# Optimization experiments

Measured on AMD Instinct MI355X. Metric: run time of the kernel, lower is better.

Reference implementation:

```python
import jax, jax.numpy as jnp
import numpy as np

N_SRC0, N_DST0, N_DST1 = 100000, 20000, 4000
E0, E1 = 640000, 128000
IN_F, HID_F, OUT_F = 512, 512, 256


def _graph_conv(x_src, src, dst, W, b, n_src, n_dst):
    """DGL GraphConv, norm='both': D_out^{-1/2} A D_in^{-1/2} X W + b."""
    ones_e = jnp.ones(src.shape[0], x_src.dtype)
    out_deg = jnp.maximum(jax.ops.segment_sum(ones_e, src, num_segments=n_src), 1.0)
    in_deg = jnp.maximum(jax.ops.segment_sum(ones_e, dst, num_segments=n_dst), 1.0)
    h = x_src * (out_deg ** -0.5)[:, None]          # [n_src, F] pre-normalize
    agg = jax.ops.segment_sum(h[src], dst, num_segments=n_dst)  # gather -> scatter-add
    agg = agg * (in_deg ** -0.5)[:, None]           # [n_dst, F]
    return agg @ W + b


def setup_inputs() -> dict:
    key = jax.random.key(0)
    ks = jax.random.split(key, 8)
    x = jax.random.normal(ks[0], (N_SRC0, IN_F), jnp.float32)
    src0 = jax.random.randint(ks[1], (E0,), 0, N_SRC0)
    dst0 = jax.random.randint(ks[2], (E0,), 0, N_DST0)
    src1 = jax.random.randint(ks[3], (E1,), 0, N_DST0)
    dst1 = jax.random.randint(ks[4], (E1,), 0, N_DST1)
    W1 = jax.random.normal(ks[5], (IN_F, HID_F), jnp.float32) * (IN_F ** -0.5)
    b1 = jnp.zeros((HID_F,), jnp.float32)
    W2 = jax.random.normal(ks[6], (HID_F, OUT_F), jnp.float32) * (HID_F ** -0.5)
    b2 = jnp.zeros((OUT_F,), jnp.float32)
    return {"x": x, "src0": src0, "dst0": dst0, "src1": src1, "dst1": dst1,
            "W1": W1, "b1": b1, "W2": W2, "b2": b2,
            "n_src0": N_SRC0, "n_dst0": N_DST0, "n_dst1": N_DST1}


def reference(x, src0, dst0, src1, dst1, W1, b1, W2, b2, n_src0, n_dst0, n_dst1):
    h = jax.nn.relu(_graph_conv(x, src0, dst0, W1, b1, n_src0, n_dst0))
    out = jax.nn.relu(_graph_conv(h, src1, dst1, W2, b2, n_dst0, n_dst1))
    return out
```

## Files before the change

### kernel.cpp

```cpp
#include <hip/hip_runtime.h>

typedef unsigned short ushort_t;
typedef unsigned int uint_t;
typedef __attribute__((ext_vector_type(8))) short s8v;
typedef __attribute__((ext_vector_type(4))) float f4v;

#define NS0 100000
#define ND0 20000
#define ND1 4000
#define E0  640000
#define E1  128000
#define F   512
#define OF  256
#define NCNT (NS0 + ND0 + ND0 + ND1)
#define SB  96

__device__ __forceinline__ ushort_t f2b(float f) {
    uint_t u = __float_as_uint(f);
    uint_t r = (u + 0x7fffu + ((u >> 16) & 1u)) >> 16;
    return (ushort_t)r;
}
__device__ __forceinline__ float b2f_lo(uint_t u) { return __uint_as_float(u << 16); }
__device__ __forceinline__ float b2f_hi(uint_t u) { return __uint_as_float(u & 0xffff0000u); }

__global__ __launch_bounds__(256) void bucket_fill(const int* __restrict__ src0, const int* __restrict__ dst0,
                                                   const int* __restrict__ src1, const int* __restrict__ dst1,
                                                   int* __restrict__ cntOut0, int* __restrict__ cntIn0,
                                                   int* __restrict__ cntOut1, int* __restrict__ cntIn1,
                                                   int* __restrict__ es0, int* __restrict__ es1) {
    int b = blockIdx.x;
    if (b < 625) {
        int e = (b * 256 + threadIdx.x) * 4;
        int4 s = *(const int4*)(src0 + e);
        int4 d = *(const int4*)(dst0 + e);
        atomicAdd(&cntOut0[s.x], 1);
        atomicAdd(&cntOut0[s.y], 1);
        atomicAdd(&cntOut0[s.z], 1);
        atomicAdd(&cntOut0[s.w], 1);
        int p0 = atomicAdd(&cntIn0[d.x], 1);
        int p1 = atomicAdd(&cntIn0[d.y], 1);
        int p2 = atomicAdd(&cntIn0[d.z], 1);
        int p3 = atomicAdd(&cntIn0[d.w], 1);
        es0[d.x * SB + min(p0, SB - 1)] = s.x;
        es0[d.y * SB + min(p1, SB - 1)] = s.y;
        es0[d.z * SB + min(p2, SB - 1)] = s.z;
        es0[d.w * SB + min(p3, SB - 1)] = s.w;
    } else {
        int e = ((b - 625) * 256 + threadIdx.x) * 4;
        int4 s = *(const int4*)(src1 + e);
        int4 d = *(const int4*)(dst1 + e);
        atomicAdd(&cntOut1[s.x], 1);
        atomicAdd(&cntOut1[s.y], 1);
        atomicAdd(&cntOut1[s.z], 1);
        atomicAdd(&cntOut1[s.w], 1);
        int p0 = atomicAdd(&cntIn1[d.x], 1);
        int p1 = atomicAdd(&cntIn1[d.y], 1);
        int p2 = atomicAdd(&cntIn1[d.z], 1);
        int p3 = atomicAdd(&cntIn1[d.w], 1);
        es1[d.x * SB + min(p0, SB - 1)] = s.x;
        es1[d.y * SB + min(p1, SB - 1)] = s.y;
        es1[d.z * SB + min(p2, SB - 1)] = s.z;
        es1[d.w * SB + min(p3, SB - 1)] = s.w;
    }
}

#define WBLK ((F * F + F * OF) / 256)
#define XBLK (NS0 * 128 / 256)
__global__ __launch_bounds__(256) void conv_wx(const float* __restrict__ W1, const float* __restrict__ W2,
                                               ushort_t* __restrict__ wt1, ushort_t* __restrict__ wt2,
                                               const float* __restrict__ x, ushort_t* __restrict__ xb) {
    if (blockIdx.x < WBLK) {
        int i = blockIdx.x * 256 + threadIdx.x;
        if (i < F * F) {
            int k = i >> 9, n = i & (F - 1);
            wt1[n * F + k] = f2b(W1[i]);
        } else {
            int j = i - F * F;
            int k = j >> 8, n = j & (OF - 1);
            wt2[n * F + k] = f2b(W2[j]);
        }
        return;
    }
    int i = (blockIdx.x - WBLK) * 256 + threadIdx.x;
    if (i >= NS0 * 128) return;
    f4v v = __builtin_nontemporal_load(((const f4v*)x) + i);
    uint2 o;
    o.x = (uint_t)f2b(v.x) | ((uint_t)f2b(v.y) << 16);
    o.y = (uint_t)f2b(v.z) | ((uint_t)f2b(v.w) << 16);
    ((uint2*)xb)[i] = o;
}

__device__ __forceinline__ void fma8(float* acc, uint4 u, float sc) {
    acc[0] += b2f_lo(u.x) * sc; acc[1] += b2f_hi(u.x) * sc;
    acc[2] += b2f_lo(u.y) * sc; acc[3] += b2f_hi(u.y) * sc;
    acc[4] += b2f_lo(u.z) * sc; acc[5] += b2f_hi(u.z) * sc;
    acc[6] += b2f_lo(u.w) * sc; acc[7] += b2f_hi(u.w) * sc;
}
__device__ __forceinline__ void add8(float* acc, uint4 u) {
    acc[0] += b2f_lo(u.x); acc[1] += b2f_hi(u.x);
    acc[2] += b2f_lo(u.y); acc[3] += b2f_hi(u.y);
    acc[4] += b2f_lo(u.z); acc[5] += b2f_hi(u.z);
    acc[6] += b2f_lo(u.w); acc[7] += b2f_hi(u.w);
}

__global__ __launch_bounds__(256) void agg_l1(const ushort_t* __restrict__ X, const int* __restrict__ es,
                                              const int* __restrict__ cntIn, const int* __restrict__ cntOut,
                                              ushort_t* __restrict__ out, int ndst) {
    int d = __builtin_amdgcn_readfirstlane(blockIdx.x * 4 + (threadIdx.x >> 6));
    if (d >= ndst) return;
    int lane = threadIdx.x & 63;
    int n = min(cntIn[d], SB);
    const int* ed = es + (size_t)d * SB;
    const uint4* Xv = (const uint4*)X;
    float acc[8] = {0.f, 0.f, 0.f, 0.f, 0.f, 0.f, 0.f, 0.f};
    int i = 0;
    for (; i + 8 <= n; i += 8) {
        int sv[8];
        #pragma unroll
        for (int j = 0; j < 8; ++j) sv[j] = ed[i + j];
        uint4 u[8];
        #pragma unroll
        for (int j = 0; j < 8; ++j) u[j] = Xv[(size_t)sv[j] * 64 + lane];
        float scv[8];
        #pragma unroll
        for (int j = 0; j < 8; ++j) scv[j] = rsqrtf(fmaxf((float)cntOut[sv[j]], 1.0f));
        #pragma unroll
        for (int j = 0; j < 8; ++j) fma8(acc, u[j], scv[j]);
    }
    for (; i < n; ++i) {
        int s = ed[i];
        float sc = rsqrtf(fmaxf((float)cntOut[s], 1.0f));
        fma8(acc, Xv[(size_t)s * 64 + lane], sc);
    }
    float sc = rsqrtf(fmaxf((float)n, 1.0f));
    uint4 o;
    o.x = (uint_t)f2b(acc[0] * sc) | ((uint_t)f2b(acc[1] * sc) << 16);
    o.y = (uint_t)f2b(acc[2] * sc) | ((uint_t)f2b(acc[3] * sc) << 16);
    o.z = (uint_t)f2b(acc[4] * sc) | ((uint_t)f2b(acc[5] * sc) << 16);
    o.w = (uint_t)f2b(acc[6] * sc) | ((uint_t)f2b(acc[7] * sc) << 16);
    ((uint4*)out)[(size_t)d * 64 + lane] = o;
}

__global__ __launch_bounds__(256) void agg_l2(const ushort_t* __restrict__ X, const int* __restrict__ es,
                                              const int* __restrict__ cntIn, ushort_t* __restrict__ out,
                                              int ndst) {
    int d = __builtin_amdgcn_readfirstlane(blockIdx.x * 4 + (threadIdx.x >> 6));
    if (d >= ndst) return;
    int lane = threadIdx.x & 63;
    int n = min(cntIn[d], SB);
    const int* ed = es + (size_t)d * SB;
    const uint4* Xv = (const uint4*)X;
    float acc[8] = {0.f, 0.f, 0.f, 0.f, 0.f, 0.f, 0.f, 0.f};
    int i = 0;
    for (; i + 16 <= n; i += 16) {
        uint4 u[16];
        #pragma unroll
        for (int j = 0; j < 16; ++j) u[j] = Xv[(size_t)ed[i + j] * 64 + lane];
        #pragma unroll
        for (int j = 0; j < 16; ++j) add8(acc, u[j]);
    }
    for (; i + 4 <= n; i += 4) {
        uint4 u[4];
        #pragma unroll
        for (int j = 0; j < 4; ++j) u[j] = Xv[(size_t)ed[i + j] * 64 + lane];
        #pragma unroll
        for (int j = 0; j < 4; ++j) add8(acc, u[j]);
    }
    for (; i < n; ++i) add8(acc, Xv[(size_t)ed[i] * 64 + lane]);
    float sc = rsqrtf(fmaxf((float)n, 1.0f));
    uint4 o;
    o.x = (uint_t)f2b(acc[0] * sc) | ((uint_t)f2b(acc[1] * sc) << 16);
    o.y = (uint_t)f2b(acc[2] * sc) | ((uint_t)f2b(acc[3] * sc) << 16);
    o.z = (uint_t)f2b(acc[4] * sc) | ((uint_t)f2b(acc[5] * sc) << 16);
    o.w = (uint_t)f2b(acc[6] * sc) | ((uint_t)f2b(acc[7] * sc) << 16);
    ((uint4*)out)[(size_t)d * 64 + lane] = o;
}

template <typename OutT>
__global__ __launch_bounds__(256) void gemm128(const ushort_t* __restrict__ A, const ushort_t* __restrict__ BT,
                                               const float* __restrict__ bias, const int* __restrict__ rowCnt,
                                               OutT* __restrict__ C, int M, int N, int K) {
    __shared__ __align__(16) ushort_t As[128 * 64];
    __shared__ __align__(16) ushort_t Bs[128 * 64];
    int tid = threadIdx.x;
    int lane = tid & 63, w = tid >> 6;
    int m16 = lane & 15, quad = lane >> 4;
    int wm = w & 1, wn = w >> 1;
    int bm = blockIdx.x * 128, bn = blockIdx.y * 128;
    f4v acc[4][4] = {};
    for (int k0 = 0; k0 < K; k0 += 64) {
        #pragma unroll
        for (int i = 0; i < 4; ++i) {
            int c = i * 256 + tid;
            int row = c >> 3, seg = (c & 7) * 8;
            int ra = bm + row; if (ra >= M) ra = M - 1;
            __builtin_amdgcn_global_load_lds(
                (const __attribute__((address_space(1))) uint_t*)(A + (size_t)ra * K + k0 + seg),
                (__attribute__((address_space(3))) uint_t*)(As + (size_t)c * 8), 16, 0, 0);
        }
        #pragma unroll
        for (int i = 0; i < 4; ++i) {
            int c = i * 256 + tid;
            int row = c >> 3, seg = (c & 7) * 8;
            int rb = bn + row;
            __builtin_amdgcn_global_load_lds(
                (const __attribute__((address_space(1))) uint_t*)(BT + (size_t)rb * K + k0 + seg),
                (__attribute__((address_space(3))) uint_t*)(Bs + (size_t)c * 8), 16, 0, 0);
        }
        __syncthreads();
        #pragma unroll
        for (int kc = 0; kc < 2; ++kc) {
            int co = kc * 32 + quad * 8;
            s8v af[4], bf[4];
            #pragma unroll
            for (int m = 0; m < 4; ++m)
                af[m] = *(const s8v*)&As[(wm * 64 + m * 16 + m16) * 64 + co];
            #pragma unroll
            for (int nn = 0; nn < 4; ++nn)
                bf[nn] = *(const s8v*)&Bs[(wn * 64 + nn * 16 + m16) * 64 + co];
            #pragma unroll
            for (int m = 0; m < 4; ++m)
                #pragma unroll
                for (int nn = 0; nn < 4; ++nn)
                    acc[m][nn] = __builtin_amdgcn_mfma_f32_16x16x32_bf16(af[m], bf[nn], acc[m][nn], 0, 0, 0);
        }
        __syncthreads();
    }
    #pragma unroll
    for (int m = 0; m < 4; ++m) {
        #pragma unroll
        for (int rr = 0; rr < 4; ++rr) {
            int row = bm + wm * 64 + m * 16 + quad * 4 + rr;
            if (row < M) {
                float rs = rowCnt ? rsqrtf(fmaxf((float)rowCnt[row], 1.0f)) : 1.0f;
                #pragma unroll
                for (int nn = 0; nn < 4; ++nn) {
                    int col = bn + wn * 64 + nn * 16 + m16;
                    float v = fmaxf(acc[m][nn][rr] + bias[col], 0.0f) * rs;
                    if (sizeof(OutT) == 2)
                        ((ushort_t*)C)[(size_t)row * N + col] = f2b(v);
                    else
                        ((float*)C)[(size_t)row * N + col] = v;
                }
            }
        }
    }
}

extern "C" void kernel_launch(void* const* d_in, const int* in_sizes, int n_in,
                              void* d_out, int out_size, void* d_ws, size_t ws_size,
                              hipStream_t stream) {
    (void)in_sizes; (void)n_in; (void)out_size; (void)ws_size;
    const float* x    = (const float*)d_in[0];
    const int*   src0 = (const int*)d_in[1];
    const int*   dst0 = (const int*)d_in[2];
    const int*   src1 = (const int*)d_in[3];
    const int*   dst1 = (const int*)d_in[4];
    const float* W1   = (const float*)d_in[5];
    const float* b1   = (const float*)d_in[6];
    const float* W2   = (const float*)d_in[7];
    const float* b2   = (const float*)d_in[8];
    float* out = (float*)d_out;

    char* p = (char*)d_ws;
    auto alloc = [&](size_t bytes) { char* q = p; p += (bytes + 255) & ~(size_t)255; return q; };
    int*      cnt  = (int*)alloc((size_t)NCNT * 4);
    int*      es0  = (int*)alloc((size_t)ND0 * SB * 4);
    int*      es1  = (int*)alloc((size_t)ND1 * SB * 4);
    ushort_t* wt1  = (ushort_t*)alloc((size_t)F * F * 2);
    ushort_t* wt2  = (ushort_t*)alloc((size_t)OF * F * 2);
    ushort_t* agg0 = (ushort_t*)alloc((size_t)ND0 * F * 2);
    ushort_t* h    = (ushort_t*)alloc((size_t)ND0 * F * 2);
    ushort_t* agg1 = (ushort_t*)alloc((size_t)ND1 * F * 2);
    ushort_t* xb   = (ushort_t*)alloc((size_t)NS0 * F * 2);

    int* cntOut0 = cnt;
    int* cntIn0  = cnt + NS0;
    int* cntOut1 = cnt + NS0 + ND0;
    int* cntIn1  = cnt + NS0 + ND0 + ND0;

    (void)hipMemsetAsync(cnt, 0, (size_t)NCNT * 4, stream);

    bucket_fill<<<750, 256, 0, stream>>>(src0, dst0, src1, dst1,
                                         cntOut0, cntIn0, cntOut1, cntIn1, es0, es1);

    conv_wx<<<WBLK + XBLK, 256, 0, stream>>>(W1, W2, wt1, wt2, x, xb);

    agg_l1<<<(ND0 + 3) / 4, 256, 0, stream>>>(xb, es0, cntIn0, cntOut0, agg0, ND0);

    gemm128<ushort_t><<<dim3((ND0 + 127) / 128, F / 128), 256, 0, stream>>>(
        agg0, wt1, b1, cntOut1, h, ND0, F, F);

    agg_l2<<<(ND1 + 3) / 4, 256, 0, stream>>>(h, es1, cntIn1, agg1, ND1);

    gemm128<float><<<dim3((ND1 + 127) / 128, OF / 128), 256, 0, stream>>>(
        agg1, wt2, b2, nullptr, out, ND1, OF, F);
}
```

Before: 532.7 us.

## Merge bucket fill and conversion kernels; prefetch next edge indices in agg_l1

Combines the edge bucketing kernel and the weight/feature bf16 conversion kernel into a single launch, so the atomic-heavy bucketing blocks and the bandwidth-bound x conversion blocks can run concurrently and one launch gap goes away. The agg_l1 main loop now loads the next 8 source indices before accumulating the current batch, which shortens the dependency between the index load and the gather. The bounds check on the x conversion was removed because the grid divides evenly. Register pressure in agg_l1 rises slightly.

```diff
diff --git a/kernel.cpp b/kernel.cpp
--- a/kernel.cpp
+++ b/kernel.cpp
@@ -15,6 +15,9 @@
 #define NCNT (NS0 + ND0 + ND0 + ND1)
 #define SB  96
 
+#define WBLK ((F * F + F * OF) / 256)
+#define XBLK (NS0 * 128 / 256)
+
 __device__ __forceinline__ ushort_t f2b(float f) {
     uint_t u = __float_as_uint(f);
     uint_t r = (u + 0x7fffu + ((u >> 16) & 1u)) >> 16;
@@ -23,11 +26,14 @@
 __device__ __forceinline__ float b2f_lo(uint_t u) { return __uint_as_float(u << 16); }
 __device__ __forceinline__ float b2f_hi(uint_t u) { return __uint_as_float(u & 0xffff0000u); }
 
-__global__ __launch_bounds__(256) void bucket_fill(const int* __restrict__ src0, const int* __restrict__ dst0,
-                                                   const int* __restrict__ src1, const int* __restrict__ dst1,
-                                                   int* __restrict__ cntOut0, int* __restrict__ cntIn0,
-                                                   int* __restrict__ cntOut1, int* __restrict__ cntIn1,
-                                                   int* __restrict__ es0, int* __restrict__ es1) {
+__global__ __launch_bounds__(256) void prep(const int* __restrict__ src0, const int* __restrict__ dst0,
+                                            const int* __restrict__ src1, const int* __restrict__ dst1,
+                                            int* __restrict__ cntOut0, int* __restrict__ cntIn0,
+                                            int* __restrict__ cntOut1, int* __restrict__ cntIn1,
+                                            int* __restrict__ es0, int* __restrict__ es1,
+                                            const float* __restrict__ W1, const float* __restrict__ W2,
+                                            ushort_t* __restrict__ wt1, ushort_t* __restrict__ wt2,
+                                            const float* __restrict__ x, ushort_t* __restrict__ xb) {
     int b = blockIdx.x;
     if (b < 625) {
         int e = (b * 256 + threadIdx.x) * 4;
@@ -45,7 +51,9 @@
         es0[d.y * SB + min(p1, SB - 1)] = s.y;
         es0[d.z * SB + min(p2, SB - 1)] = s.z;
         es0[d.w * SB + min(p3, SB - 1)] = s.w;
-    } else {
+        return;
+    }
+    if (b < 750) {
         int e = ((b - 625) * 256 + threadIdx.x) * 4;
         int4 s = *(const int4*)(src1 + e);
         int4 d = *(const int4*)(dst1 + e);
@@ -61,16 +69,11 @@
         es1[d.y * SB + min(p1, SB - 1)] = s.y;
         es1[d.z * SB + min(p2, SB - 1)] = s.z;
         es1[d.w * SB + min(p3, SB - 1)] = s.w;
-    }
-}
-
-#define WBLK ((F * F + F * OF) / 256)
-#define XBLK (NS0 * 128 / 256)
-__global__ __launch_bounds__(256) void conv_wx(const float* __restrict__ W1, const float* __restrict__ W2,
-                                               ushort_t* __restrict__ wt1, ushort_t* __restrict__ wt2,
-                                               const float* __restrict__ x, ushort_t* __restrict__ xb) {
-    if (blockIdx.x < WBLK) {
-        int i = blockIdx.x * 256 + threadIdx.x;
+        return;
+    }
+    int bb = b - 750;
+    if (bb < WBLK) {
+        int i = bb * 256 + threadIdx.x;
         if (i < F * F) {
             int k = i >> 9, n = i & (F - 1);
             wt1[n * F + k] = f2b(W1[i]);
@@ -81,8 +84,7 @@
         }
         return;
     }
-    int i = (blockIdx.x - WBLK) * 256 + threadIdx.x;
-    if (i >= NS0 * 128) return;
+    int i = (bb - WBLK) * 256 + threadIdx.x;
     f4v v = __builtin_nontemporal_load(((const f4v*)x) + i);
     uint2 o;
     o.x = (uint_t)f2b(v.x) | ((uint_t)f2b(v.y) << 16);
@@ -114,18 +116,33 @@
     const uint4* Xv = (const uint4*)X;
     float acc[8] = {0.f, 0.f, 0.f, 0.f, 0.f, 0.f, 0.f, 0.f};
     int i = 0;
-    for (; i + 8 <= n; i += 8) {
+    int nb = n & ~7;
+    if (nb) {
         int sv[8];
         #pragma unroll
-        for (int j = 0; j < 8; ++j) sv[j] = ed[i + j];
-        uint4 u[8];
-        #pragma unroll
-        for (int j = 0; j < 8; ++j) u[j] = Xv[(size_t)sv[j] * 64 + lane];
-        float scv[8];
-        #pragma unroll
-        for (int j = 0; j < 8; ++j) scv[j] = rsqrtf(fmaxf((float)cntOut[sv[j]], 1.0f));
-        #pragma unroll
-        for (int j = 0; j < 8; ++j) fma8(acc, u[j], scv[j]);
+        for (int j = 0; j < 8; ++j) sv[j] = ed[j];
+        while (true) {
+            uint4 u[8];
+            #pragma unroll
+            for (int j = 0; j < 8; ++j) u[j] = Xv[(size_t)sv[j] * 64 + lane];
+            float scv[8];
+            #pragma unroll
+            for (int j = 0; j < 8; ++j) scv[j] = rsqrtf(fmaxf((float)cntOut[sv[j]], 1.0f));
+            i += 8;
+            if (i < nb) {
+                int sn[8];
+                #pragma unroll
+                for (int j = 0; j < 8; ++j) sn[j] = ed[i + j];
+                #pragma unroll
+                for (int j = 0; j < 8; ++j) fma8(acc, u[j], scv[j]);
+                #pragma unroll
+                for (int j = 0; j < 8; ++j) sv[j] = sn[j];
+            } else {
+                #pragma unroll
+                for (int j = 0; j < 8; ++j) fma8(acc, u[j], scv[j]);
+                break;
+            }
+        }
     }
     for (; i < n; ++i) {
         int s = ed[i];
@@ -281,10 +298,9 @@
 
     (void)hipMemsetAsync(cnt, 0, (size_t)NCNT * 4, stream);
 
-    bucket_fill<<<750, 256, 0, stream>>>(src0, dst0, src1, dst1,
-                                         cntOut0, cntIn0, cntOut1, cntIn1, es0, es1);
-
-    conv_wx<<<WBLK + XBLK, 256, 0, stream>>>(W1, W2, wt1, wt2, x, xb);
+    prep<<<750 + WBLK + XBLK, 256, 0, stream>>>(src0, dst0, src1, dst1,
+                                                cntOut0, cntIn0, cntOut1, cntIn1, es0, es1,
+                                                W1, W2, wt1, wt2, x, xb);
 
     agg_l1<<<(ND0 + 3) / 4, 256, 0, stream>>>(xb, es0, cntIn0, cntOut0, agg0, ND0);
 
```

Measured after the change: 524.5 us. About the same (-1.5%).
